# Performance work log

Measured on AMD Instinct MI355X. Metric: run time of the kernel, lower is better.

Reference implementation:

```python
import jax, jax.numpy as jnp
import numpy as np

B, L, D = 4, 4096, 1024
S, H, DH = 256, 16, 64
TOPK = 8
NEG_INF = float('-inf')


def setup_inputs() -> dict:
    key = jax.random.key(0)
    ks = jax.random.split(key, 10)
    scale = 1.0 / np.sqrt(D)
    return {
        'token_states': jax.random.normal(ks[0], (B, L, D), dtype=jnp.float32),
        'Z_sets': jax.random.normal(ks[1], (B, S, H, DH), dtype=jnp.float32),
        'desc_q': jax.random.normal(ks[2], (B, S, D), dtype=jnp.float32),
        'mask_q': jnp.ones((B, S), dtype=bool),
        'Wg_w': jax.random.normal(ks[3], (D, D), dtype=jnp.float32) * scale,
        'Wg_b': jnp.zeros((D,), dtype=jnp.float32),
        'Wd_w': jax.random.normal(ks[4], (D, D), dtype=jnp.float32) * scale,
        'Wd_b': jnp.zeros((D,), dtype=jnp.float32),
        'out_w': jax.random.normal(ks[5], (D, D), dtype=jnp.float32) * scale,
        'out_b': jnp.zeros((D,), dtype=jnp.float32),
    }


def reference(token_states, Z_sets, desc_q, mask_q, Wg_w, Wg_b, Wd_w, Wd_b, out_w, out_b):
    # torch nn.Linear: y = x @ W.T + b
    Tproj = token_states @ Wg_w.T + Wg_b          # (B,L,D)
    Dproj = desc_q @ Wd_w.T + Wd_b                # (B,S,D)
    logits = jnp.einsum('bld,bsd->bls', Tproj, Dproj)  # (B,L,S)
    logits = jnp.where(mask_q[:, None, :], logits, NEG_INF)
    if TOPK > 0 and S > TOPK:
        vals, idx = jax.lax.top_k(logits, TOPK)   # (B,L,K)
        probs = jax.nn.softmax(vals, axis=-1)     # softmax over the K kept logits
        b_ix = jnp.arange(B)[:, None, None]
        l_ix = jnp.arange(L)[None, :, None]
        G = jnp.zeros_like(logits).at[b_ix, l_ix, idx].set(probs)
    else:
        G = jax.nn.softmax(logits, axis=-1)
    mix = jnp.einsum('bls,bshd->blhd', G, Z_sets)  # (B,L,H,DH)
    return mix.reshape(B, L, D) @ out_w.T + out_b
```

## Files before the change

### kernel.cpp

```cpp
#include <hip/hip_runtime.h>
#include <hip/hip_bf16.h>
#include <stdint.h>


#define B_ 4
#define L_ 4096
#define D_ 1024
#define S_ 256

typedef short s16x8 __attribute__((ext_vector_type(8)));
typedef _Float16 f16x8 __attribute__((ext_vector_type(8)));
typedef float f32x4 __attribute__((ext_vector_type(4)));

__device__ __forceinline__ unsigned short f2bf(float f) {
  uint32_t u = __float_as_uint(f);
  u += 0x7FFFu + ((u >> 16) & 1u);
  return (unsigned short)(u >> 16);
}
__device__ __forceinline__ float bf2f(unsigned short h) {
  return __uint_as_float(((uint32_t)h) << 16);
}
__device__ __forceinline__ unsigned short f2h(float f) {
  _Float16 h = (_Float16)f;
  return __builtin_bit_cast(unsigned short, h);
}
__device__ __forceinline__ int kperm32(int k5) {
  return (((k5 >> 2) & 3) << 3) | (((k5 >> 4) & 1) << 2) | (k5 & 3);
}

__global__ __launch_bounds__(256)
void prep_all(const float* __restrict__ desc, const float* __restrict__ Zf,
              const float* __restrict__ Wd, const float* __restrict__ oW,
              const float* __restrict__ Wg,
              unsigned short* __restrict__ dHi, unsigned short* __restrict__ dLo,
              unsigned short* __restrict__ zHi,
              unsigned short* __restrict__ wdHi, unsigned short* __restrict__ wdLo,
              unsigned short* __restrict__ owHi,
              unsigned short* __restrict__ wgTHi, unsigned short* __restrict__ wgTLo) {
  __shared__ float t[64][65];
  const int bid = blockIdx.x, tid = threadIdx.x;
  if (bid < 4096) {
    const float* src[4] = {desc, Zf, Wd, oW};
    unsigned short* hi[4] = {dHi, zHi, wdHi, owHi};
    unsigned short* lo[4] = {dLo, nullptr, wdLo, nullptr};
    int job = bid >> 10;
    int i = (bid & 1023) * 256 + tid;
    float4 v = reinterpret_cast<const float4*>(src[job])[i];
    int idx = i << 2;
    int nidx = (idx & ~31) | (((idx >> 2) & 3) << 3) | (((idx >> 4) & 1) << 2);
    float a[4] = {v.x, v.y, v.z, v.w};
    unsigned short hb[4];
#pragma unroll
    for (int e = 0; e < 4; ++e) hb[e] = f2bf(a[e]);
    *reinterpret_cast<ushort4*>(hi[job] + nidx) = make_ushort4(hb[0], hb[1], hb[2], hb[3]);
    if (lo[job]) {
      unsigned short lb[4];
#pragma unroll
      for (int e = 0; e < 4; ++e) lb[e] = f2bf(a[e] - bf2f(hb[e]));
      *reinterpret_cast<ushort4*>(lo[job] + nidx) = make_ushort4(lb[0], lb[1], lb[2], lb[3]);
    }
  } else {
    int tb = bid - 4096;
    int bx = tb & 15, by = tb >> 4;
    int c = tid & 63, r0 = tid >> 6;
#pragma unroll
    for (int rr = 0; rr < 16; ++rr) {
      int r = r0 * 16 + rr;
      t[r][c] = Wg[(size_t)(by * 64 + r) * 1024 + bx * 64 + c];
    }
    __syncthreads();
#pragma unroll
    for (int rr = 0; rr < 16; ++rr) {
      int r = r0 * 16 + rr;
      float v = t[c][r];
      int kcol = by * 64 + (c & 32) + kperm32(c & 31);
      size_t o = (size_t)(bx * 64 + r) * 1024 + kcol;
      unsigned short hb = f2bf(v);
      wgTHi[o] = hb;
      wgTLo[o] = f2bf(v - bf2f(hb));
    }
  }
}

__global__ __launch_bounds__(256, 2)
void gemm_a(const unsigned short* __restrict__ dHi, const unsigned short* __restrict__ dLo,
            const unsigned short* __restrict__ wdHi, const unsigned short* __restrict__ wdLo,
            const unsigned short* __restrict__ zHi, const unsigned short* __restrict__ owHi,
            float* __restrict__ P) {
  __shared__ unsigned short lAh[128 * 64], lAl[128 * 64];
  __shared__ unsigned short lBh[128 * 64], lBl[128 * 64];
  const int tid = threadIdx.x;
  const int w = tid >> 6, l = tid & 63;
  const int g = l >> 4, r15 = l & 15;
  const int rowBase = blockIdx.y * 128, colBase = blockIdx.x * 128;
  const int prob = blockIdx.z >> 2, kz = blockIdx.z & 3;
  const bool t3 = (prob == 0);
  const unsigned short* Ah = t3 ? dHi : zHi;
  const unsigned short* Bh = t3 ? wdHi : owHi;
  const int wr = (w >> 1) * 64, wc = (w & 1) * 64;
  const int k0 = kz * 256;

  f32x4 acc[4][4] = {};

  for (int kt = k0; kt < k0 + 256; kt += 64) {
    __syncthreads();
#pragma unroll
    for (int j = 0; j < 4; ++j) {
      int cl = j * 256 + tid;
      int r = cl >> 3;
      int c16 = (cl & 7) ^ (r & 7);
      long ao = (long)(rowBase + r) * 1024 + kt + c16 * 8;
      long bo = (long)(colBase + r) * 1024 + kt + c16 * 8;
      size_t doff = (size_t)(j * 256 + w * 64) * 8;
      __builtin_amdgcn_global_load_lds((const __attribute__((address_space(1))) void*)(Ah + ao),
                                       (__attribute__((address_space(3))) void*)(lAh + doff), 16, 0, 0);
      __builtin_amdgcn_global_load_lds((const __attribute__((address_space(1))) void*)(Bh + bo),
                                       (__attribute__((address_space(3))) void*)(lBh + doff), 16, 0, 0);
      if (t3) {
        __builtin_amdgcn_global_load_lds((const __attribute__((address_space(1))) void*)(dLo + ao),
                                         (__attribute__((address_space(3))) void*)(lAl + doff), 16, 0, 0);
        __builtin_amdgcn_global_load_lds((const __attribute__((address_space(1))) void*)(wdLo + bo),
                                         (__attribute__((address_space(3))) void*)(lBl + doff), 16, 0, 0);
      }
    }
    __syncthreads();
#pragma unroll
    for (int ks = 0; ks < 2; ++ks) {
      s16x8 ah[4], bh[4];
#pragma unroll
      for (int m = 0; m < 4; ++m) {
        int row = wr + m * 16 + r15;
        int offb = (row * 128 + ks * 64 + g * 16) ^ ((row & 7) << 4);
        ah[m] = *reinterpret_cast<const s16x8*>(reinterpret_cast<const char*>(lAh) + offb);
      }
#pragma unroll
      for (int n = 0; n < 4; ++n) {
        int row = wc + n * 16 + r15;
        int offb = (row * 128 + ks * 64 + g * 16) ^ ((row & 7) << 4);
        bh[n] = *reinterpret_cast<const s16x8*>(reinterpret_cast<const char*>(lBh) + offb);
      }
#pragma unroll
      for (int m = 0; m < 4; ++m)
#pragma unroll
        for (int n = 0; n < 4; ++n)
          acc[m][n] = __builtin_amdgcn_mfma_f32_16x16x32_bf16(ah[m], bh[n], acc[m][n], 0, 0, 0);
      if (t3) {
        s16x8 al[4], bl[4];
#pragma unroll
        for (int m = 0; m < 4; ++m) {
          int row = wr + m * 16 + r15;
          int offb = (row * 128 + ks * 64 + g * 16) ^ ((row & 7) << 4);
          al[m] = *reinterpret_cast<const s16x8*>(reinterpret_cast<const char*>(lAl) + offb);
        }
#pragma unroll
        for (int n = 0; n < 4; ++n) {
          int row = wc + n * 16 + r15;
          int offb = (row * 128 + ks * 64 + g * 16) ^ ((row & 7) << 4);
          bl[n] = *reinterpret_cast<const s16x8*>(reinterpret_cast<const char*>(lBl) + offb);
        }
#pragma unroll
        for (int m = 0; m < 4; ++m)
#pragma unroll
          for (int n = 0; n < 4; ++n) {
            acc[m][n] = __builtin_amdgcn_mfma_f32_16x16x32_bf16(al[m], bh[n], acc[m][n], 0, 0, 0);
            acc[m][n] = __builtin_amdgcn_mfma_f32_16x16x32_bf16(ah[m], bl[n], acc[m][n], 0, 0, 0);
          }
      }
    }
  }

  float* Cz = P + (long)blockIdx.z * (1 << 20);
#pragma unroll
  for (int m = 0; m < 4; ++m)
#pragma unroll
    for (int n = 0; n < 4; ++n) {
      int col = colBase + wc + n * 16 + r15;
#pragma unroll
      for (int q = 0; q < 4; ++q) {
        int row = rowBase + wr + m * 16 + g * 4 + q;
        Cz[(long)row * 1024 + col] = acc[m][n][q];
      }
    }
}

__global__ __launch_bounds__(256, 2)
void gemm_f3(const unsigned short* __restrict__ Ahi, const unsigned short* __restrict__ Alo,
             const unsigned short* __restrict__ Bhi, const unsigned short* __restrict__ Blo,
             float* __restrict__ C) {
  __shared__ unsigned short lAh[128 * 64], lAl[128 * 64];
  __shared__ unsigned short lBh[128 * 64], lBl[128 * 64];
  const int tid = threadIdx.x;
  const int w = tid >> 6, l = tid & 63;
  const int g = l >> 4, r15 = l & 15;
  const int rowBase = blockIdx.y * 128, colBase = blockIdx.x * 128;
  const int kz = blockIdx.z;
  const int wr = (w >> 1) * 64, wc = (w & 1) * 64;
  const int k0 = kz * 128;

  f32x4 acc[4][4] = {};

  for (int kt = k0; kt < k0 + 128; kt += 64) {
    __syncthreads();
#pragma unroll
    for (int j = 0; j < 4; ++j) {
      int cl = j * 256 + tid;
      int r = cl >> 3;
      int c16 = (cl & 7) ^ (r & 7);
      long ao = (long)(rowBase + r) * 1024 + kt + c16 * 8;
      long bo = (long)(colBase + r) * 1024 + kt + c16 * 8;
      size_t doff = (size_t)(j * 256 + w * 64) * 8;
      __builtin_amdgcn_global_load_lds((const __attribute__((address_space(1))) void*)(Ahi + ao),
                                       (__attribute__((address_space(3))) void*)(lAh + doff), 16, 0, 0);
      __builtin_amdgcn_global_load_lds((const __attribute__((address_space(1))) void*)(Alo + ao),
                                       (__attribute__((address_space(3))) void*)(lAl + doff), 16, 0, 0);
      __builtin_amdgcn_global_load_lds((const __attribute__((address_space(1))) void*)(Bhi + bo),
                                       (__attribute__((address_space(3))) void*)(lBh + doff), 16, 0, 0);
      __builtin_amdgcn_global_load_lds((const __attribute__((address_space(1))) void*)(Blo + bo),
                                       (__attribute__((address_space(3))) void*)(lBl + doff), 16, 0, 0);
    }
    __syncthreads();
#pragma unroll
    for (int ks = 0; ks < 2; ++ks) {
      s16x8 ah[4], al[4], bh[4], bl[4];
#pragma unroll
      for (int m = 0; m < 4; ++m) {
        int row = wr + m * 16 + r15;
        int offb = (row * 128 + ks * 64 + g * 16) ^ ((row & 7) << 4);
        ah[m] = *reinterpret_cast<const s16x8*>(reinterpret_cast<const char*>(lAh) + offb);
        al[m] = *reinterpret_cast<const s16x8*>(reinterpret_cast<const char*>(lAl) + offb);
      }
#pragma unroll
      for (int n = 0; n < 4; ++n) {
        int row = wc + n * 16 + r15;
        int offb = (row * 128 + ks * 64 + g * 16) ^ ((row & 7) << 4);
        bh[n] = *reinterpret_cast<const s16x8*>(reinterpret_cast<const char*>(lBh) + offb);
        bl[n] = *reinterpret_cast<const s16x8*>(reinterpret_cast<const char*>(lBl) + offb);
      }
#pragma unroll
      for (int m = 0; m < 4; ++m)
#pragma unroll
        for (int n = 0; n < 4; ++n) {
          acc[m][n] = __builtin_amdgcn_mfma_f32_16x16x32_bf16(ah[m], bh[n], acc[m][n], 0, 0, 0);
          acc[m][n] = __builtin_amdgcn_mfma_f32_16x16x32_bf16(al[m], bh[n], acc[m][n], 0, 0, 0);
          acc[m][n] = __builtin_amdgcn_mfma_f32_16x16x32_bf16(ah[m], bl[n], acc[m][n], 0, 0, 0);
        }
    }
  }

  float* Cz = C + (long)blockIdx.z * (1 << 20);
#pragma unroll
  for (int m = 0; m < 4; ++m)
#pragma unroll
    for (int n = 0; n < 4; ++n) {
      int col = colBase + wc + n * 16 + r15;
#pragma unroll
      for (int q = 0; q < 4; ++q) {
        int row = rowBase + wr + m * 16 + g * 4 + q;
        Cz[(long)row * 1024 + col] = acc[m][n][q];
      }
    }
}

__global__ __launch_bounds__(256)
void post_a(const float* __restrict__ P, const float* __restrict__ Wd_b,
            const float* __restrict__ out_b, const float* __restrict__ Wg_b,
            unsigned short* __restrict__ dpHi, unsigned short* __restrict__ dpLo,
            unsigned short* __restrict__ zwB, float* __restrict__ cb) {
  int w = threadIdx.x >> 6, l = threadIdx.x & 63;
  int job = blockIdx.x;
  if (job < 256) {
    int row = job * 4 + w;
    const float* r0 = P + (size_t)row * 1024;
    float s = 0.f;
#pragma unroll
    for (int j = 0; j < 4; ++j) {
      int i = j * 64 + l;
      float4 a0 = reinterpret_cast<const float4*>(r0)[i];
      float4 a1 = reinterpret_cast<const float4*>(r0 + (1 << 20))[i];
      float4 a2 = reinterpret_cast<const float4*>(r0 + 2 * (1 << 20))[i];
      float4 a3 = reinterpret_cast<const float4*>(r0 + 3 * (1 << 20))[i];
      float4 bb = reinterpret_cast<const float4*>(Wd_b)[i & 255];
      float4 v = make_float4(a0.x + a1.x + a2.x + a3.x + bb.x,
                             a0.y + a1.y + a2.y + a3.y + bb.y,
                             a0.z + a1.z + a2.z + a3.z + bb.z,
                             a0.w + a1.w + a2.w + a3.w + bb.w);
      float4 g = reinterpret_cast<const float4*>(Wg_b)[i & 255];
      s += v.x * g.x + v.y * g.y + v.z * g.z + v.w * g.w;
      int idx = i << 2;
      int nidx = (idx & ~31) | (((idx >> 2) & 3) << 3) | (((idx >> 4) & 1) << 2);
      float arr[4] = {v.x, v.y, v.z, v.w};
      unsigned short hb[4], lb[4];
#pragma unroll
      for (int e = 0; e < 4; ++e) {
        hb[e] = f2bf(arr[e]);
        lb[e] = f2bf(arr[e] - bf2f(hb[e]));
      }
      *reinterpret_cast<ushort4*>(dpHi + (size_t)row * 1024 + nidx) =
          make_ushort4(hb[0], hb[1], hb[2], hb[3]);
      *reinterpret_cast<ushort4*>(dpLo + (size_t)row * 1024 + nidx) =
          make_ushort4(lb[0], lb[1], lb[2], lb[3]);
    }
#pragma unroll
    for (int off = 32; off; off >>= 1) s += __shfl_xor(s, off);
    if (l == 0) cb[row] = s;
  } else {
    int row = (job - 256) * 4 + w;
    const float* r0 = P + 4 * (1 << 20) + (size_t)row * 1024;
#pragma unroll
    for (int j = 0; j < 4; ++j) {
      int i = j * 64 + l;
      float4 a0 = reinterpret_cast<const float4*>(r0)[i];
      float4 a1 = reinterpret_cast<const float4*>(r0 + (1 << 20))[i];
      float4 a2 = reinterpret_cast<const float4*>(r0 + 2 * (1 << 20))[i];
      float4 a3 = reinterpret_cast<const float4*>(r0 + 3 * (1 << 20))[i];
      float4 bb = reinterpret_cast<const float4*>(out_b)[i & 255];
      *reinterpret_cast<ushort4*>(zwB + (size_t)row * 1024 + (i << 2)) =
          make_ushort4(f2bf(a0.x + a1.x + a2.x + a3.x + bb.x),
                       f2bf(a0.y + a1.y + a2.y + a3.y + bb.y),
                       f2bf(a0.z + a1.z + a2.z + a3.z + bb.z),
                       f2bf(a0.w + a1.w + a2.w + a3.w + bb.w));
    }
  }
}

__global__ __launch_bounds__(256)
void post_mt(const float* __restrict__ P, unsigned short* __restrict__ mtF16) {
  int w = threadIdx.x >> 6, l = threadIdx.x & 63;
  int row = blockIdx.x * 4 + w;
  const float* r0 = P + (size_t)row * 1024;
#pragma unroll
  for (int j = 0; j < 4; ++j) {
    int i = j * 64 + l;
    float sx = 0.f, sy = 0.f, sz = 0.f, sw = 0.f;
#pragma unroll
    for (int p = 0; p < 8; ++p) {
      float4 a = reinterpret_cast<const float4*>(r0 + (size_t)p * (1 << 20))[i];
      sx += a.x; sy += a.y; sz += a.z; sw += a.w;
    }
    int idx = i << 2;
    int nidx = (idx & ~31) | (((idx >> 2) & 3) << 3) | (((idx >> 4) & 1) << 2);
    *reinterpret_cast<ushort4*>(mtF16 + (size_t)row * 1024 + nidx) =
        make_ushort4(f2h(sx), f2h(sy), f2h(sz), f2h(sw));
  }
}

template <int KSPLIT>
__global__ __launch_bounds__(256, 2)
void gemm_af32(const float* __restrict__ A,
               const unsigned short* __restrict__ Bh16,
               float* __restrict__ Ct, int K,
               long batchA, long batchB, long batchCt, long kzStrideCt) {
  __shared__ unsigned short lAh[128 * 64];
  __shared__ unsigned short lBh[128 * 64];
  const int tid = threadIdx.x;
  const int w = tid >> 6, l = tid & 63;
  const int g = l >> 4, r15 = l & 15;
  const int nwg = gridDim.x * gridDim.y * gridDim.z;
  int h = blockIdx.x + gridDim.x * (blockIdx.y + gridDim.y * blockIdx.z);
  int lg = (h % 8) * (nwg / 8) + h / 8;
  const int bx = lg % gridDim.x;
  const int by = (lg / gridDim.x) % gridDim.y;
  const int bzz = lg / (gridDim.x * gridDim.y);
  const int rowBase = by * 128, colBase = bx * 128;
  const int bz = bzz / KSPLIT, kz = bzz % KSPLIT;
  const long zA = (long)bz * batchA, zB = (long)bz * batchB;
  const int wr = (w >> 1) * 64, wc = (w & 1) * 64;
  const int chunk = K / KSPLIT, k0 = kz * chunk;

  f32x4 acc[4][4] = {};

  for (int kt = k0; kt < k0 + chunk; kt += 64) {
    float4 av[8];
#pragma unroll
    for (int j = 0; j < 8; ++j) {
      int cl = j * 256 + tid;
      int r = cl >> 4, k4 = cl & 15;
      av[j] = *reinterpret_cast<const float4*>(A + zA + (long)(rowBase + r) * K + kt + k4 * 4);
    }
    __syncthreads();
#pragma unroll
    for (int j = 0; j < 4; ++j) {
      int cl = j * 256 + tid;
      int r = cl >> 3;
      int c16 = (cl & 7) ^ (r & 7);
      long bo = zB + (long)(colBase + r) * K + kt + c16 * 8;
      size_t doff = (size_t)(j * 256 + w * 64) * 8;
      __builtin_amdgcn_global_load_lds((const __attribute__((address_space(1))) void*)(Bh16 + bo),
                                       (__attribute__((address_space(3))) void*)(lBh + doff), 16, 0, 0);
    }
#pragma unroll
    for (int j = 0; j < 8; ++j) {
      int cl = j * 256 + tid;
      int r = cl >> 4, k4 = cl & 15;
      int byteoff = r * 128 + ((k4 >> 3) << 6) + ((k4 & 3) << 4) + (((k4 >> 2) & 1) << 3);
      int swz = byteoff ^ ((r & 7) << 4);
      *reinterpret_cast<ushort4*>(reinterpret_cast<char*>(lAh) + swz) =
          make_ushort4(f2h(av[j].x), f2h(av[j].y), f2h(av[j].z), f2h(av[j].w));
    }
    __syncthreads();
#pragma unroll
    for (int ks = 0; ks < 2; ++ks) {
      f16x8 ah[4], bh[4];
#pragma unroll
      for (int m = 0; m < 4; ++m) {
        int row = wr + m * 16 + r15;
        int offb = (row * 128 + ks * 64 + g * 16) ^ ((row & 7) << 4);
        ah[m] = *reinterpret_cast<const f16x8*>(reinterpret_cast<const char*>(lAh) + offb);
      }
#pragma unroll
      for (int n = 0; n < 4; ++n) {
        int row = wc + n * 16 + r15;
        int offb = (row * 128 + ks * 64 + g * 16) ^ ((row & 7) << 4);
        bh[n] = *reinterpret_cast<const f16x8*>(reinterpret_cast<const char*>(lBh) + offb);
      }
#pragma unroll
      for (int m = 0; m < 4; ++m)
#pragma unroll
        for (int n = 0; n < 4; ++n)
          acc[m][n] = __builtin_amdgcn_mfma_f32_16x16x32_f16(ah[m], bh[n], acc[m][n], 0, 0, 0);
    }
  }

  float* Cz = Ct + kz * kzStrideCt + (long)bz * batchCt;
#pragma unroll
  for (int m = 0; m < 4; ++m)
#pragma unroll
    for (int n = 0; n < 4; ++n) {
      int col = colBase + wc + n * 16 + r15;
      int row0 = rowBase + wr + m * 16 + g * 4;
      *reinterpret_cast<float4*>(Cz + (long)col * L_ + row0) =
          make_float4(acc[m][n][0], acc[m][n][1], acc[m][n][2], acc[m][n][3]);
    }
}

__global__ __launch_bounds__(64)
void topk8_k(const float* __restrict__ lt, const float* __restrict__ cb,
             int* __restrict__ tokIdx, float* __restrict__ tokP) {
  int t = blockIdx.x * 64 + threadIdx.x;
  int b = t >> 12, l = t & 4095;
  const float* p0 = lt + (long)b * (256 * 4096) + l;
  const float* p1 = p0 + (1 << 22);
  const float* cbb = cb + b * 256;
  uint32_t v0 = 0, v1 = 0, v2 = 0, v3 = 0, v4 = 0, v5 = 0, v6 = 0, v7 = 0;
  auto loadb = [&](float* dst, int s0) {
#pragma unroll
    for (int u = 0; u < 8; ++u) {
      long o = (long)(s0 + u) * 4096;
      dst[u] = p0[o] + p1[o] + cbb[s0 + u];
    }
  };
  auto insert = [&](const float* val, int s0) {
#pragma unroll
    for (int u = 0; u < 8; ++u) {
      uint32_t iu = __float_as_uint(val[u]);
      uint32_t x = (iu ^ ((uint32_t)((int)iu >> 31) | 0x80000000u));
      x = (x & 0xFFFFFF00u) | (uint32_t)(255 - (s0 + u));
      uint32_t w0 = (x > v1) ? v1 : (x > v0 ? x : v0);
      uint32_t w1 = (x > v2) ? v2 : (x > v1 ? x : v1);
      uint32_t w2 = (x > v3) ? v3 : (x > v2 ? x : v2);
      uint32_t w3 = (x > v4) ? v4 : (x > v3 ? x : v3);
      uint32_t w4 = (x > v5) ? v5 : (x > v4 ? x : v4);
      uint32_t w5 = (x > v6) ? v6 : (x > v5 ? x : v5);
      uint32_t w6 = (x > v7) ? v7 : (x > v6 ? x : v6);
      uint32_t w7 = (x > v7) ? x : v7;
      v0 = w0; v1 = w1; v2 = w2; v3 = w3; v4 = w4; v5 = w5; v6 = w6; v7 = w7;
    }
  };
  float va[8], vb[8];
  loadb(va, 0);
  for (int s0 = 0; s0 < 256; s0 += 16) {
    loadb(vb, s0 + 8);
    insert(va, s0);
    if (s0 + 16 < 256) loadb(va, s0 + 16);
    insert(vb, s0 + 8);
  }
  uint32_t keys[8] = {v0, v1, v2, v3, v4, v5, v6, v7};
  float vals[8];
  int sidx[8];
#pragma unroll
  for (int i = 0; i < 8; ++i) {
    int s = 255 - (int)(keys[i] & 255u);
    sidx[i] = s;
    long o = (long)s * 4096;
    vals[i] = p0[o] + p1[o] + cbb[s];
  }
  float m = vals[0];
#pragma unroll
  for (int i = 1; i < 8; ++i) m = fmaxf(m, vals[i]);
  float p[8], ssum = 0.f;
#pragma unroll
  for (int i = 0; i < 8; ++i) { p[i] = __expf(vals[i] - m); ssum += p[i]; }
  float inv = 1.f / ssum;
#pragma unroll
  for (int i = 0; i < 8; ++i) {
    tokIdx[(long)t * 8 + i] = b * 256 + sidx[i];
    tokP[(long)t * 8 + i] = p[i] * inv;
  }
}

__global__ __launch_bounds__(256)
void mix_k(const int* __restrict__ tokIdx, const float* __restrict__ tokP,
           const unsigned short* __restrict__ zwB, float* __restrict__ out) {
  int w = threadIdx.x >> 6, l = threadIdx.x & 63;
  long t = (long)blockIdx.x * 4 + w;
  int ridx[8];
  float wt[8];
#pragma unroll
  for (int i = 0; i < 8; ++i) {
    ridx[i] = tokIdx[t * 8 + i];
    wt[i] = tokP[t * 8 + i];
  }
  float acc[16] = {};
#pragma unroll
  for (int i = 0; i < 8; ++i) {
    const unsigned short* zr = zwB + (long)ridx[i] * 1024 + l * 16;
    uint4 q0 = *reinterpret_cast<const uint4*>(zr);
    uint4 q1 = *reinterpret_cast<const uint4*>(zr + 8);
    uint32_t qs[8] = {q0.x, q0.y, q0.z, q0.w, q1.x, q1.y, q1.z, q1.w};
#pragma unroll
    for (int e = 0; e < 8; ++e) {
      acc[e * 2]     += wt[i] * __uint_as_float(qs[e] << 16);
      acc[e * 2 + 1] += wt[i] * __uint_as_float(qs[e] & 0xFFFF0000u);
    }
  }
  float* orow = out + t * 1024 + l * 16;
#pragma unroll
  for (int j = 0; j < 4; ++j)
    reinterpret_cast<float4*>(orow)[j] =
        make_float4(acc[j * 4], acc[j * 4 + 1], acc[j * 4 + 2], acc[j * 4 + 3]);
}

extern "C" void kernel_launch(void* const* d_in, const int* in_sizes, int n_in,
                              void* d_out, int out_size, void* d_ws, size_t ws_size,
                              hipStream_t stream) {
  const float* token = (const float*)d_in[0];
  const float* Z     = (const float*)d_in[1];
  const float* descq = (const float*)d_in[2];
  const float* Wg    = (const float*)d_in[4];
  const float* Wg_b  = (const float*)d_in[5];
  const float* Wd    = (const float*)d_in[6];
  const float* Wd_b  = (const float*)d_in[7];
  const float* outW  = (const float*)d_in[8];
  const float* out_b = (const float*)d_in[9];
  float* out = (float*)d_out;
  (void)in_sizes; (void)n_in; (void)out_size; (void)ws_size;

  char* ws = (char*)d_ws;
  const size_t MB = 1u << 20;
  unsigned short* dHi   = (unsigned short*)(ws + 0 * MB);
  unsigned short* dLo   = (unsigned short*)(ws + 2 * MB);
  unsigned short* wdHi  = (unsigned short*)(ws + 4 * MB);
  unsigned short* wdLo  = (unsigned short*)(ws + 6 * MB);
  unsigned short* zHi   = (unsigned short*)(ws + 8 * MB);
  unsigned short* owHi  = (unsigned short*)(ws + 10 * MB);
  unsigned short* wgTHi = (unsigned short*)(ws + 12 * MB);
  unsigned short* wgTLo = (unsigned short*)(ws + 14 * MB);
  float*          P     = (float*)         (ws + 16 * MB);
  unsigned short* dpHi  = (unsigned short*)(ws + 0 * MB);
  unsigned short* dpLo  = (unsigned short*)(ws + 2 * MB);
  unsigned short* mtF16 = (unsigned short*)(ws + 4 * MB);
  unsigned short* zwB   = (unsigned short*)(ws + 8 * MB);
  float*          cb    = (float*)         (ws + 10 * MB);
  int*            tokIdx= (int*)           (ws + 10 * MB + 512 * 1024);
  float*          tokP  = (float*)         (ws + 11 * MB);
  float*          lt    = (float*)         (ws + 16 * MB);

  prep_all<<<4352, 256, 0, stream>>>(descq, Z, Wd, outW, Wg,
                                     dHi, dLo, zHi, wdHi, wdLo, owHi,
                                     wgTHi, wgTLo);

  gemm_a<<<dim3(8, 8, 8), 256, 0, stream>>>(dHi, dLo, wdHi, wdLo, zHi, owHi, P);

  post_a<<<512, 256, 0, stream>>>(P, Wd_b, out_b, Wg_b, dpHi, dpLo, zwB, cb);

  gemm_f3<<<dim3(8, 8, 8), 256, 0, stream>>>(dpHi, dpLo, wgTHi, wgTLo, P);

  post_mt<<<256, 256, 0, stream>>>(P, mtF16);

  gemm_af32<2><<<dim3(2, 32, 8), 256, 0, stream>>>(token, mtF16, lt, 1024,
                                                   (long)L_ * D_, (long)S_ * D_,
                                                   (long)L_ * S_, 4194304L);

  topk8_k<<<256, 64, 0, stream>>>(lt, cb, tokIdx, tokP);

  mix_k<<<4096, 256, 0, stream>>>(tokIdx, tokP, zwB, out);
}
```

Measured before the change: 132.7 us.

## Fuse logits GEMM with top-8 selection and softmax in one kernel

Replaces the split-K logits GEMM and the separate top-k kernel with one kernel. Each block computes a 32-token by 256-slot logit tile, adds the bias in LDS and runs the top-8 selection and softmax there. This removes the split-K partial logits round trip through global memory and one launch. In exchange, each block holds all 256 columns of B in LDS, uses more LDS, drops split-K, and runs the top-k scan on only 32 of 256 threads, which can leave the selection phase serialized.

```diff
diff --git a/kernel.cpp b/kernel.cpp
--- a/kernel.cpp
+++ b/kernel.cpp
@@ -344,157 +344,136 @@
   }
 }
 
-template <int KSPLIT>
 __global__ __launch_bounds__(256, 2)
-void gemm_af32(const float* __restrict__ A,
-               const unsigned short* __restrict__ Bh16,
-               float* __restrict__ Ct, int K,
-               long batchA, long batchB, long batchCt, long kzStrideCt) {
-  __shared__ unsigned short lAh[128 * 64];
-  __shared__ unsigned short lBh[128 * 64];
+void gemm_topk(const float* __restrict__ A, const unsigned short* __restrict__ Bh16,
+               const float* __restrict__ cb,
+               int* __restrict__ tokIdx, float* __restrict__ tokP) {
+  __shared__ unsigned short lA[32 * 64];
+  __shared__ unsigned short lB[256 * 64];
+  __shared__ float lgs[32][257];
+  __shared__ float lcb[256];
   const int tid = threadIdx.x;
   const int w = tid >> 6, l = tid & 63;
   const int g = l >> 4, r15 = l & 15;
-  const int nwg = gridDim.x * gridDim.y * gridDim.z;
-  int h = blockIdx.x + gridDim.x * (blockIdx.y + gridDim.y * blockIdx.z);
-  int lg = (h % 8) * (nwg / 8) + h / 8;
-  const int bx = lg % gridDim.x;
-  const int by = (lg / gridDim.x) % gridDim.y;
-  const int bzz = lg / (gridDim.x * gridDim.y);
-  const int rowBase = by * 128, colBase = bx * 128;
-  const int bz = bzz / KSPLIT, kz = bzz % KSPLIT;
-  const long zA = (long)bz * batchA, zB = (long)bz * batchB;
-  const int wr = (w >> 1) * 64, wc = (w & 1) * 64;
-  const int chunk = K / KSPLIT, k0 = kz * chunk;
-
-  f32x4 acc[4][4] = {};
-
-  for (int kt = k0; kt < k0 + chunk; kt += 64) {
-    float4 av[8];
-#pragma unroll
-    for (int j = 0; j < 8; ++j) {
+  int h = blockIdx.x;
+  int lg = (h & 7) * 64 + (h >> 3);
+  const int rowBase = lg * 32;
+  const int batch = rowBase >> 12;
+  const long zA = (long)rowBase * 1024;
+  const long zB = (long)batch * (256 * 1024);
+  lcb[tid] = cb[batch * 256 + tid];
+
+  f32x4 acc[2][4] = {};
+
+  for (int kt = 0; kt < 1024; kt += 64) {
+    float4 av[2];
+#pragma unroll
+    for (int j = 0; j < 2; ++j) {
       int cl = j * 256 + tid;
       int r = cl >> 4, k4 = cl & 15;
-      av[j] = *reinterpret_cast<const float4*>(A + zA + (long)(rowBase + r) * K + kt + k4 * 4);
-    }
-    __syncthreads();
-#pragma unroll
-    for (int j = 0; j < 4; ++j) {
+      av[j] = *reinterpret_cast<const float4*>(A + zA + (long)r * 1024 + kt + k4 * 4);
+    }
+    __syncthreads();
+#pragma unroll
+    for (int j = 0; j < 8; ++j) {
       int cl = j * 256 + tid;
       int r = cl >> 3;
       int c16 = (cl & 7) ^ (r & 7);
-      long bo = zB + (long)(colBase + r) * K + kt + c16 * 8;
+      long bo = zB + (long)r * 1024 + kt + c16 * 8;
       size_t doff = (size_t)(j * 256 + w * 64) * 8;
       __builtin_amdgcn_global_load_lds((const __attribute__((address_space(1))) void*)(Bh16 + bo),
-                                       (__attribute__((address_space(3))) void*)(lBh + doff), 16, 0, 0);
-    }
-#pragma unroll
-    for (int j = 0; j < 8; ++j) {
+                                       (__attribute__((address_space(3))) void*)(lB + doff), 16, 0, 0);
+    }
+#pragma unroll
+    for (int j = 0; j < 2; ++j) {
       int cl = j * 256 + tid;
       int r = cl >> 4, k4 = cl & 15;
       int byteoff = r * 128 + ((k4 >> 3) << 6) + ((k4 & 3) << 4) + (((k4 >> 2) & 1) << 3);
       int swz = byteoff ^ ((r & 7) << 4);
-      *reinterpret_cast<ushort4*>(reinterpret_cast<char*>(lAh) + swz) =
+      *reinterpret_cast<ushort4*>(reinterpret_cast<char*>(lA) + swz) =
           make_ushort4(f2h(av[j].x), f2h(av[j].y), f2h(av[j].z), f2h(av[j].w));
     }
     __syncthreads();
 #pragma unroll
     for (int ks = 0; ks < 2; ++ks) {
-      f16x8 ah[4], bh[4];
-#pragma unroll
-      for (int m = 0; m < 4; ++m) {
-        int row = wr + m * 16 + r15;
+      f16x8 ah[2], bh[4];
+#pragma unroll
+      for (int m = 0; m < 2; ++m) {
+        int row = m * 16 + r15;
         int offb = (row * 128 + ks * 64 + g * 16) ^ ((row & 7) << 4);
-        ah[m] = *reinterpret_cast<const f16x8*>(reinterpret_cast<const char*>(lAh) + offb);
+        ah[m] = *reinterpret_cast<const f16x8*>(reinterpret_cast<const char*>(lA) + offb);
       }
 #pragma unroll
       for (int n = 0; n < 4; ++n) {
-        int row = wc + n * 16 + r15;
+        int row = w * 64 + n * 16 + r15;
         int offb = (row * 128 + ks * 64 + g * 16) ^ ((row & 7) << 4);
-        bh[n] = *reinterpret_cast<const f16x8*>(reinterpret_cast<const char*>(lBh) + offb);
-      }
-#pragma unroll
-      for (int m = 0; m < 4; ++m)
+        bh[n] = *reinterpret_cast<const f16x8*>(reinterpret_cast<const char*>(lB) + offb);
+      }
+#pragma unroll
+      for (int m = 0; m < 2; ++m)
 #pragma unroll
         for (int n = 0; n < 4; ++n)
           acc[m][n] = __builtin_amdgcn_mfma_f32_16x16x32_f16(ah[m], bh[n], acc[m][n], 0, 0, 0);
     }
   }
 
-  float* Cz = Ct + kz * kzStrideCt + (long)bz * batchCt;
-#pragma unroll
-  for (int m = 0; m < 4; ++m)
+  __syncthreads();
+#pragma unroll
+  for (int m = 0; m < 2; ++m)
 #pragma unroll
     for (int n = 0; n < 4; ++n) {
-      int col = colBase + wc + n * 16 + r15;
-      int row0 = rowBase + wr + m * 16 + g * 4;
-      *reinterpret_cast<float4*>(Cz + (long)col * L_ + row0) =
-          make_float4(acc[m][n][0], acc[m][n][1], acc[m][n][2], acc[m][n][3]);
-    }
-}
-
-__global__ __launch_bounds__(64)
-void topk8_k(const float* __restrict__ lt, const float* __restrict__ cb,
-             int* __restrict__ tokIdx, float* __restrict__ tokP) {
-  int t = blockIdx.x * 64 + threadIdx.x;
-  int b = t >> 12, l = t & 4095;
-  const float* p0 = lt + (long)b * (256 * 4096) + l;
-  const float* p1 = p0 + (1 << 22);
-  const float* cbb = cb + b * 256;
-  uint32_t v0 = 0, v1 = 0, v2 = 0, v3 = 0, v4 = 0, v5 = 0, v6 = 0, v7 = 0;
-  auto loadb = [&](float* dst, int s0) {
-#pragma unroll
-    for (int u = 0; u < 8; ++u) {
-      long o = (long)(s0 + u) * 4096;
-      dst[u] = p0[o] + p1[o] + cbb[s0 + u];
-    }
-  };
-  auto insert = [&](const float* val, int s0) {
-#pragma unroll
-    for (int u = 0; u < 8; ++u) {
-      uint32_t iu = __float_as_uint(val[u]);
-      uint32_t x = (iu ^ ((uint32_t)((int)iu >> 31) | 0x80000000u));
-      x = (x & 0xFFFFFF00u) | (uint32_t)(255 - (s0 + u));
-      uint32_t w0 = (x > v1) ? v1 : (x > v0 ? x : v0);
-      uint32_t w1 = (x > v2) ? v2 : (x > v1 ? x : v1);
-      uint32_t w2 = (x > v3) ? v3 : (x > v2 ? x : v2);
-      uint32_t w3 = (x > v4) ? v4 : (x > v3 ? x : v3);
-      uint32_t w4 = (x > v5) ? v5 : (x > v4 ? x : v4);
-      uint32_t w5 = (x > v6) ? v6 : (x > v5 ? x : v5);
-      uint32_t w6 = (x > v7) ? v7 : (x > v6 ? x : v6);
-      uint32_t w7 = (x > v7) ? x : v7;
-      v0 = w0; v1 = w1; v2 = w2; v3 = w3; v4 = w4; v5 = w5; v6 = w6; v7 = w7;
-    }
-  };
-  float va[8], vb[8];
-  loadb(va, 0);
-  for (int s0 = 0; s0 < 256; s0 += 16) {
-    loadb(vb, s0 + 8);
-    insert(va, s0);
-    if (s0 + 16 < 256) loadb(va, s0 + 16);
-    insert(vb, s0 + 8);
-  }
-  uint32_t keys[8] = {v0, v1, v2, v3, v4, v5, v6, v7};
-  float vals[8];
-  int sidx[8];
-#pragma unroll
-  for (int i = 0; i < 8; ++i) {
-    int s = 255 - (int)(keys[i] & 255u);
-    sidx[i] = s;
-    long o = (long)s * 4096;
-    vals[i] = p0[o] + p1[o] + cbb[s];
-  }
-  float m = vals[0];
-#pragma unroll
-  for (int i = 1; i < 8; ++i) m = fmaxf(m, vals[i]);
-  float p[8], ssum = 0.f;
-#pragma unroll
-  for (int i = 0; i < 8; ++i) { p[i] = __expf(vals[i] - m); ssum += p[i]; }
-  float inv = 1.f / ssum;
-#pragma unroll
-  for (int i = 0; i < 8; ++i) {
-    tokIdx[(long)t * 8 + i] = b * 256 + sidx[i];
-    tokP[(long)t * 8 + i] = p[i] * inv;
+      int col = w * 64 + n * 16 + r15;
+#pragma unroll
+      for (int q = 0; q < 4; ++q) {
+        int rloc = m * 16 + g * 4 + q;
+        lgs[rloc][col] = acc[m][n][q] + lcb[col];
+      }
+    }
+  __syncthreads();
+
+  if (tid < 32) {
+    int row = tid;
+    uint32_t v0 = 0, v1 = 0, v2 = 0, v3 = 0, v4 = 0, v5 = 0, v6 = 0, v7 = 0;
+    for (int s0 = 0; s0 < 256; s0 += 8) {
+#pragma unroll
+      for (int u = 0; u < 8; ++u) {
+        float val = lgs[row][s0 + u];
+        uint32_t iu = __float_as_uint(val);
+        uint32_t x = (iu ^ ((uint32_t)((int)iu >> 31) | 0x80000000u));
+        x = (x & 0xFFFFFF00u) | (uint32_t)(255 - (s0 + u));
+        uint32_t w0 = (x > v1) ? v1 : (x > v0 ? x : v0);
+        uint32_t w1 = (x > v2) ? v2 : (x > v1 ? x : v1);
+        uint32_t w2 = (x > v3) ? v3 : (x > v2 ? x : v2);
+        uint32_t w3 = (x > v4) ? v4 : (x > v3 ? x : v3);
+        uint32_t w4 = (x > v5) ? v5 : (x > v4 ? x : v4);
+        uint32_t w5 = (x > v6) ? v6 : (x > v5 ? x : v5);
+        uint32_t w6 = (x > v7) ? v7 : (x > v6 ? x : v6);
+        uint32_t w7 = (x > v7) ? x : v7;
+        v0 = w0; v1 = w1; v2 = w2; v3 = w3; v4 = w4; v5 = w5; v6 = w6; v7 = w7;
+      }
+    }
+    uint32_t keys[8] = {v0, v1, v2, v3, v4, v5, v6, v7};
+    float vals[8];
+    int sidx[8];
+#pragma unroll
+    for (int i = 0; i < 8; ++i) {
+      int s = 255 - (int)(keys[i] & 255u);
+      sidx[i] = s;
+      vals[i] = lgs[row][s];
+    }
+    float m = vals[0];
+#pragma unroll
+    for (int i = 1; i < 8; ++i) m = fmaxf(m, vals[i]);
+    float p[8], ssum = 0.f;
+#pragma unroll
+    for (int i = 0; i < 8; ++i) { p[i] = __expf(vals[i] - m); ssum += p[i]; }
+    float inv = 1.f / ssum;
+    long t = rowBase + row;
+#pragma unroll
+    for (int i = 0; i < 8; ++i) {
+      tokIdx[t * 8 + i] = batch * 256 + sidx[i];
+      tokP[t * 8 + i] = p[i] * inv;
+    }
   }
 }
 
@@ -563,7 +542,6 @@
   float*          cb    = (float*)         (ws + 10 * MB);
   int*            tokIdx= (int*)           (ws + 10 * MB + 512 * 1024);
   float*          tokP  = (float*)         (ws + 11 * MB);
-  float*          lt    = (float*)         (ws + 16 * MB);
 
   prep_all<<<4352, 256, 0, stream>>>(descq, Z, Wd, outW, Wg,
                                      dHi, dLo, zHi, wdHi, wdLo, owHi,
@@ -577,11 +555,7 @@
 
   post_mt<<<256, 256, 0, stream>>>(P, mtF16);
 
-  gemm_af32<2><<<dim3(2, 32, 8), 256, 0, stream>>>(token, mtF16, lt, 1024,
-                                                   (long)L_ * D_, (long)S_ * D_,
-                                                   (long)L_ * S_, 4194304L);
-
-  topk8_k<<<256, 64, 0, stream>>>(lt, cb, tokIdx, tokP);
+  gemm_topk<<<512, 256, 0, stream>>>(token, mtF16, cb, tokIdx, tokP);
 
   mix_k<<<4096, 256, 0, stream>>>(tokIdx, tokP, zwB, out);
 }
```

After: 115.8 us. 1.15x faster.

## Split top-8 selection across four lane segments with shuffle merge

Applied to the files above, without the earlier changes.

The top-k kernel now gives each token four threads instead of one. Each thread scans 64 of the 256 logits, and the four partial top-8 lists are merged with two xor-shuffle rounds, with one lane per token doing the softmax and the writes. The aim is four times as many waves, so the serial, latency-bound scan is hidden better on a launch that only had 256 single-wave blocks. In exchange, each load now covers 16 consecutive tokens instead of 64, so coalescing is narrower, and the merge adds extra compare work.

```diff
diff --git a/kernel.cpp b/kernel.cpp
--- a/kernel.cpp
+++ b/kernel.cpp
@@ -433,68 +433,86 @@
     }
 }
 
-__global__ __launch_bounds__(64)
+__global__ __launch_bounds__(256)
 void topk8_k(const float* __restrict__ lt, const float* __restrict__ cb,
              int* __restrict__ tokIdx, float* __restrict__ tokP) {
-  int t = blockIdx.x * 64 + threadIdx.x;
-  int b = t >> 12, l = t & 4095;
-  const float* p0 = lt + (long)b * (256 * 4096) + l;
+  const int tid = threadIdx.x;
+  const int w = tid >> 6, l = tid & 63;
+  const int seg = l >> 4, t16 = l & 15;
+  const long t = (long)blockIdx.x * 64 + w * 16 + t16;
+  const int b = (int)(t >> 12);
+  const float* p0 = lt + (long)b * (256 * 4096) + (t & 4095);
   const float* p1 = p0 + (1 << 22);
   const float* cbb = cb + b * 256;
+  const int sBase = seg * 64;
+
   uint32_t v0 = 0, v1 = 0, v2 = 0, v3 = 0, v4 = 0, v5 = 0, v6 = 0, v7 = 0;
-  auto loadb = [&](float* dst, int s0) {
-#pragma unroll
-    for (int u = 0; u < 8; ++u) {
-      long o = (long)(s0 + u) * 4096;
-      dst[u] = p0[o] + p1[o] + cbb[s0 + u];
-    }
+  auto insert = [&](uint32_t x) {
+    uint32_t w0 = (x > v1) ? v1 : (x > v0 ? x : v0);
+    uint32_t w1 = (x > v2) ? v2 : (x > v1 ? x : v1);
+    uint32_t w2 = (x > v3) ? v3 : (x > v2 ? x : v2);
+    uint32_t w3 = (x > v4) ? v4 : (x > v3 ? x : v3);
+    uint32_t w4 = (x > v5) ? v5 : (x > v4 ? x : v4);
+    uint32_t w5 = (x > v6) ? v6 : (x > v5 ? x : v5);
+    uint32_t w6 = (x > v7) ? v7 : (x > v6 ? x : v6);
+    uint32_t w7 = (x > v7) ? x : v7;
+    v0 = w0; v1 = w1; v2 = w2; v3 = w3; v4 = w4; v5 = w5; v6 = w6; v7 = w7;
   };
-  auto insert = [&](const float* val, int s0) {
-#pragma unroll
-    for (int u = 0; u < 8; ++u) {
-      uint32_t iu = __float_as_uint(val[u]);
-      uint32_t x = (iu ^ ((uint32_t)((int)iu >> 31) | 0x80000000u));
-      x = (x & 0xFFFFFF00u) | (uint32_t)(255 - (s0 + u));
-      uint32_t w0 = (x > v1) ? v1 : (x > v0 ? x : v0);
-      uint32_t w1 = (x > v2) ? v2 : (x > v1 ? x : v1);
-      uint32_t w2 = (x > v3) ? v3 : (x > v2 ? x : v2);
-      uint32_t w3 = (x > v4) ? v4 : (x > v3 ? x : v3);
-      uint32_t w4 = (x > v5) ? v5 : (x > v4 ? x : v4);
-      uint32_t w5 = (x > v6) ? v6 : (x > v5 ? x : v5);
-      uint32_t w6 = (x > v7) ? v7 : (x > v6 ? x : v6);
-      uint32_t w7 = (x > v7) ? x : v7;
-      v0 = w0; v1 = w1; v2 = w2; v3 = w3; v4 = w4; v5 = w5; v6 = w6; v7 = w7;
-    }
+  auto key = [&](float val, int s) {
+    uint32_t iu = __float_as_uint(val);
+    uint32_t x = (iu ^ ((uint32_t)((int)iu >> 31) | 0x80000000u));
+    return (x & 0xFFFFFF00u) | (uint32_t)(255 - s);
   };
   float va[8], vb[8];
+  auto loadb = [&](float* dst, int u0) {
+#pragma unroll
+    for (int u = 0; u < 8; ++u) {
+      long o = (long)(sBase + u0 + u) * 4096;
+      dst[u] = p0[o] + p1[o] + cbb[sBase + u0 + u];
+    }
+  };
   loadb(va, 0);
-  for (int s0 = 0; s0 < 256; s0 += 16) {
-    loadb(vb, s0 + 8);
-    insert(va, s0);
-    if (s0 + 16 < 256) loadb(va, s0 + 16);
-    insert(vb, s0 + 8);
-  }
-  uint32_t keys[8] = {v0, v1, v2, v3, v4, v5, v6, v7};
-  float vals[8];
-  int sidx[8];
-#pragma unroll
-  for (int i = 0; i < 8; ++i) {
-    int s = 255 - (int)(keys[i] & 255u);
-    sidx[i] = s;
-    long o = (long)s * 4096;
-    vals[i] = p0[o] + p1[o] + cbb[s];
-  }
-  float m = vals[0];
-#pragma unroll
-  for (int i = 1; i < 8; ++i) m = fmaxf(m, vals[i]);
-  float p[8], ssum = 0.f;
-#pragma unroll
-  for (int i = 0; i < 8; ++i) { p[i] = __expf(vals[i] - m); ssum += p[i]; }
-  float inv = 1.f / ssum;
-#pragma unroll
-  for (int i = 0; i < 8; ++i) {
-    tokIdx[(long)t * 8 + i] = b * 256 + sidx[i];
-    tokP[(long)t * 8 + i] = p[i] * inv;
+  for (int u0 = 0; u0 < 64; u0 += 16) {
+    loadb(vb, u0 + 8);
+#pragma unroll
+    for (int u = 0; u < 8; ++u) insert(key(va[u], sBase + u0 + u));
+    if (u0 + 16 < 64) loadb(va, u0 + 16);
+#pragma unroll
+    for (int u = 0; u < 8; ++u) insert(key(vb[u], sBase + u0 + 8 + u));
+  }
+#pragma unroll
+  for (int off = 16; off <= 32; off <<= 1) {
+    uint32_t k0 = v0, k1 = v1, k2 = v2, k3 = v3, k4 = v4, k5 = v5, k6 = v6, k7 = v7;
+    uint32_t f0 = __shfl_xor((int)k0, off), f1 = __shfl_xor((int)k1, off);
+    uint32_t f2 = __shfl_xor((int)k2, off), f3 = __shfl_xor((int)k3, off);
+    uint32_t f4 = __shfl_xor((int)k4, off), f5 = __shfl_xor((int)k5, off);
+    uint32_t f6 = __shfl_xor((int)k6, off), f7 = __shfl_xor((int)k7, off);
+    insert(f0); insert(f1); insert(f2); insert(f3);
+    insert(f4); insert(f5); insert(f6); insert(f7);
+  }
+  if (seg == 0) {
+    uint32_t keys[8] = {v0, v1, v2, v3, v4, v5, v6, v7};
+    float vals[8];
+    int sidx[8];
+#pragma unroll
+    for (int i = 0; i < 8; ++i) {
+      int s = 255 - (int)(keys[i] & 255u);
+      sidx[i] = s;
+      long o = (long)s * 4096;
+      vals[i] = p0[o] + p1[o] + cbb[s];
+    }
+    float m = vals[0];
+#pragma unroll
+    for (int i = 1; i < 8; ++i) m = fmaxf(m, vals[i]);
+    float p[8], ssum = 0.f;
+#pragma unroll
+    for (int i = 0; i < 8; ++i) { p[i] = __expf(vals[i] - m); ssum += p[i]; }
+    float inv = 1.f / ssum;
+#pragma unroll
+    for (int i = 0; i < 8; ++i) {
+      tokIdx[t * 8 + i] = b * 256 + sidx[i];
+      tokP[t * 8 + i] = p[i] * inv;
+    }
   }
 }
 
@@ -581,7 +599,7 @@
                                                    (long)L_ * D_, (long)S_ * D_,
                                                    (long)L_ * S_, 4194304L);
 
-  topk8_k<<<256, 64, 0, stream>>>(lt, cb, tokIdx, tokP);
+  topk8_k<<<256, 256, 0, stream>>>(lt, cb, tokIdx, tokP);
 
   mix_k<<<4096, 256, 0, stream>>>(tokIdx, tokP, zwB, out);
 }
```

New measurement: 115.5 us. 1.15x faster.
